# Optimization experiments

Hardware: AMD Instinct MI355X
Metric: run time of the kernel (lower is better)

## Reference

```python
import jax, jax.numpy as jnp
import numpy as np

B, S, H, NH, HD = 2, 2048, 2048, 16, 128
MASK_VALUE = -1e10


def setup_inputs() -> dict:
    key = jax.random.key(0)
    ks = jax.random.split(key, 5)
    scale = 1.0 / np.sqrt(H)
    x = jax.random.normal(ks[0], (B, S, H), dtype=jnp.float32)
    Wq = jax.random.normal(ks[1], (H, NH * HD), dtype=jnp.float32) * scale
    Wk = jax.random.normal(ks[2], (H, NH * HD), dtype=jnp.float32) * scale
    Wv = jax.random.normal(ks[3], (H, NH * HD), dtype=jnp.float32) * scale
    Wo = jax.random.normal(ks[4], (NH * HD, H), dtype=jnp.float32) * scale
    # causal boolean mask (B, S, S) as in decoder-style gemma usage
    mask = jnp.broadcast_to(jnp.tril(jnp.ones((S, S), dtype=bool)), (B, S, S))
    return {"x": x, "mask": mask, "Wq": Wq, "Wk": Wk, "Wv": Wv, "Wo": Wo}


def reference(x, mask, Wq, Wk, Wv, Wo):
    b, s, h = x.shape
    # bias-free QKV projections, split into heads -> (b, nh, s, hd)
    def split_heads(y):
        return y.reshape(b, s, NH, HD).transpose(0, 2, 1, 3)
    q = split_heads(x @ Wq)
    k = split_heads(x @ Wk)
    v = split_heads(x @ Wv)
    scores = jnp.einsum('bhtd,bhTd->bhtT', q, k) / jnp.sqrt(jnp.asarray(HD, x.dtype))
    scores = jnp.where(mask[:, None, :, :], scores, MASK_VALUE)
    weights = jax.nn.softmax(scores, axis=-1)
    out = jnp.einsum('bhtT,bhTd->bhtd', weights, v)
    out = out.transpose(0, 2, 1, 3).reshape(b, s, NH * HD)
    return out @ Wo
```

## Files before the change

kernel.cpp:

```cpp
#include <hip/hip_runtime.h>
#include <hip/hip_bf16.h>
#include <stdint.h>

#define DEVFN __device__ __forceinline__

typedef __attribute__((ext_vector_type(8))) short short8;
typedef __attribute__((ext_vector_type(4))) float f32x4;
typedef __attribute__((ext_vector_type(16))) float f32x16;

constexpr int S_LEN = 2048;
constexpr int HDIM  = 2048;
constexpr int NHEAD = 16;
constexpr int HD    = 128;

DEVFN unsigned short f2bf(float f){
  union { float f; unsigned u; } x; x.f = f;
  unsigned r = x.u + 0x7fffu + ((x.u >> 16) & 1u);
  return (unsigned short)(r >> 16);
}

typedef const __attribute__((address_space(1))) void* gas1_ptr;
typedef __attribute__((address_space(3))) void* las3_ptr;

DEVFN void gl_lds16(const void* g, void* l){
  __builtin_amdgcn_global_load_lds((gas1_ptr)g, (las3_ptr)l, 16, 0, 0);
}

DEVFN f32x4 mfma16(short8 a, short8 b, f32x4 c){
  return __builtin_amdgcn_mfma_f32_16x16x32_bf16(a, b, c, 0, 0, 0);
}

DEVFN f32x16 mfma32(short8 a, short8 b, f32x16 c){
  return __builtin_amdgcn_mfma_f32_32x32x16_bf16(a, b, c, 0, 0, 0);
}

DEVFN unsigned cvtpk_bf16(float lo, float hi){
  unsigned w;
  asm("v_cvt_pk_bf16_f32 %0, %1, %2" : "=v"(w) : "v"(lo), "v"(hi));
  return w;
}


__global__ void cast_x_kernel(const float* __restrict__ in, unsigned short* __restrict__ out){
  int i = (blockIdx.x * 256 + threadIdx.x) * 8;
  float4 a = *(const float4*)(in + i);
  float4 b = *(const float4*)(in + i + 4);
  union { unsigned short s[8]; short8 v; } o;
  o.s[0] = f2bf(a.x); o.s[1] = f2bf(a.y); o.s[2] = f2bf(a.z); o.s[3] = f2bf(a.w);
  o.s[4] = f2bf(b.x); o.s[5] = f2bf(b.y); o.s[6] = f2bf(b.z); o.s[7] = f2bf(b.w);
  *(short8*)(out + i) = o.v;
}

__global__ void transpose_cast_w4(const float* __restrict__ w0, const float* __restrict__ w1,
                                  const float* __restrict__ w2, const float* __restrict__ w3,
                                  unsigned short* __restrict__ out){
  __shared__ float tile[64][65];
  const int tid = threadIdx.x;
  const int kb = blockIdx.x * 64, nb = blockIdx.y * 64, z = blockIdx.z;
  const float* in = (z == 0) ? w0 : (z == 1) ? w1 : (z == 2) ? w2 : w3;
  unsigned short* op = out + (size_t)z * HDIM * HDIM;

  const int rr = tid >> 5;
  const int cc = (tid & 31) * 2;
  #pragma unroll
  for (int i = 0; i < 8; i++){
    int r = i*8 + rr;
    float2 v = *(const float2*)(in + (size_t)(kb + r) * HDIM + nb + cc);
    tile[r][cc]   = v.x;
    tile[r][cc+1] = v.y;
  }
  __syncthreads();
  #pragma unroll
  for (int p = 0; p < 2; p++){
    int task = p*256 + tid;
    int n_l = task >> 3;
    int k8  = (task & 7) * 8;
    union { unsigned short s[8]; short8 v; } o;
    #pragma unroll
    for (int j = 0; j < 8; j++)
      o.s[j] = f2bf(tile[k8 + j][n_l]);
    *(short8*)(op + (size_t)(nb + n_l) * HDIM + kb + k8) = o.v;
  }
}


DEVFN void gemm_core_bt(const unsigned short* __restrict__ A,
                        const unsigned short* __restrict__ Bt,
                        int K, int m0, int n0, char* ls, f32x4 (&acc)[4][4]){
  const int t = threadIdx.x;
  const int wid = t >> 6, lane = t & 63;
  const int wr = wid >> 1, wc = wid & 1;
  const int l15 = lane & 15, lg = lane >> 4;
  char* lsA = ls;
  char* lsB = ls + 16384;

  for (int k0 = 0; k0 < K; k0 += 64){
    __syncthreads();
    #pragma unroll
    for (int i = 0; i < 4; i++){
      int o = (t + i*256) * 16;
      int row = o >> 7;
      int col = (o & 127) ^ ((row & 7) << 4);
      gl_lds16((const char*)A + ((size_t)(m0 + row) * K + k0) * 2 + col, lsA + o);
    }
    #pragma unroll
    for (int i = 0; i < 4; i++){
      int o = (t + i*256) * 16;
      int row = o >> 7;
      int col = (o & 127) ^ ((row & 7) << 4);
      gl_lds16((const char*)Bt + ((size_t)(n0 + row) * K + k0) * 2 + col, lsB + o);
    }
    __syncthreads();
    #pragma unroll
    for (int kk = 0; kk < 2; kk++){
      short8 af[4], bfr[4];
      #pragma unroll
      for (int i = 0; i < 4; i++){
        int ra = wr*64 + i*16 + l15;
        af[i]  = *(const short8*)(lsA + ra*128 + ((kk*64 + lg*16) ^ ((ra & 7) << 4)));
        int rb = wc*64 + i*16 + l15;
        bfr[i] = *(const short8*)(lsB + rb*128 + ((kk*64 + lg*16) ^ ((rb & 7) << 4)));
      }
      #pragma unroll
      for (int i = 0; i < 4; i++)
        #pragma unroll
        for (int j = 0; j < 4; j++)
          acc[i][j] = mfma16(af[i], bfr[j], acc[i][j]);
    }
  }
}

__global__ __launch_bounds__(256, 4)
void gemm_qkv(const unsigned short* __restrict__ xb, const unsigned short* __restrict__ Wt,
              unsigned short* __restrict__ Qb, unsigned short* __restrict__ Kb,
              unsigned short* __restrict__ Vt){
  __shared__ __align__(16) char ls[32768];
  f32x4 acc[4][4];
  const f32x4 z4 = {0.f, 0.f, 0.f, 0.f};
  #pragma unroll
  for (int i = 0; i < 4; i++)
    #pragma unroll
    for (int j = 0; j < 4; j++) acc[i][j] = z4;

  const int m0 = blockIdx.x * 128;
  const int n0 = blockIdx.y * 128;
  gemm_core_bt(xb, Wt, HDIM, m0, n0, ls, acc);

  const float qscale = 0.08838834764831845f * 1.4426950408889634f;
  const int t = threadIdx.x, wid = t >> 6, lane = t & 63;
  const int wr = wid >> 1, wc = wid & 1, l15 = lane & 15, lg = lane >> 4;
  const int bb = m0 >> 11, ss0 = m0 & 2047;

  if (n0 < 4096){
    unsigned short* base = (n0 < 2048) ? Qb : Kb;
    const float sc = (n0 < 2048) ? qscale : 1.0f;
    #pragma unroll
    for (int j = 0; j < 4; j++){
      int n = n0 + wc*64 + j*16 + l15;
      int hh = (n >> 7) & 15, d = n & 127;
      #pragma unroll
      for (int i = 0; i < 4; i++){
        #pragma unroll
        for (int r = 0; r < 4; r++){
          int ss = ss0 + wr*64 + i*16 + lg*4 + r;
          base[(((size_t)bb * NHEAD + hh) * S_LEN + ss) * HD + d] = f2bf(acc[i][j][r] * sc);
        }
      }
    }
  } else {
    const int hh = (n0 - 4096) >> 7;
    __syncthreads();
    #pragma unroll
    for (int j = 0; j < 4; j++){
      int nn = wc*64 + j*16 + l15;
      #pragma unroll
      for (int i = 0; i < 4; i++){
        int mmb = (wr*64 + i*16 + lg*4) * 2;
        unsigned w0 = cvtpk_bf16(acc[i][j][0], acc[i][j][1]);
        unsigned w1 = cvtpk_bf16(acc[i][j][2], acc[i][j][3]);
        *(unsigned*)(ls + nn*256 + ((mmb    ) ^ ((nn & 7) << 4))) = w0;
        *(unsigned*)(ls + nn*256 + ((mmb + 4) ^ ((nn & 7) << 4))) = w1;
      }
    }
    __syncthreads();
    unsigned short* vout = Vt + (((size_t)bb * NHEAD + hh) * HD) * S_LEN;
    #pragma unroll
    for (int p = 0; p < 8; p++){
      int idx = p*256 + t;
      int d = idx >> 4;
      int m8 = (idx & 15) * 8;
      short8 v = *(const short8*)(ls + d*256 + ((m8*2) ^ ((d & 7) << 4)));
      *(short8*)(vout + (size_t)d * S_LEN + ss0 + m8) = v;
    }
  }
}

__global__ __launch_bounds__(256, 4)
void gemm_out(const unsigned short* __restrict__ Ob, const unsigned short* __restrict__ Wot,
              float* __restrict__ out){
  __shared__ __align__(16) char ls[32768];
  f32x4 acc[4][4];
  const f32x4 z4 = {0.f, 0.f, 0.f, 0.f};
  #pragma unroll
  for (int i = 0; i < 4; i++)
    #pragma unroll
    for (int j = 0; j < 4; j++) acc[i][j] = z4;

  const int m0 = blockIdx.x * 128;
  const int n0 = blockIdx.y * 128;
  gemm_core_bt(Ob, Wot, HDIM, m0, n0, ls, acc);

  const int t = threadIdx.x, wid = t >> 6, lane = t & 63;
  const int wr = wid >> 1, wc = wid & 1, l15 = lane & 15, lg = lane >> 4;
  #pragma unroll
  for (int i = 0; i < 4; i++){
    #pragma unroll
    for (int r = 0; r < 4; r++){
      int m = m0 + wr*64 + i*16 + lg*4 + r;
      #pragma unroll
      for (int j = 0; j < 4; j++){
        int n = n0 + wc*64 + j*16 + l15;
        out[(size_t)m * HDIM + n] = acc[i][j][r];
      }
    }
  }
}

__global__ __launch_bounds__(256, 2)
void attn_kernel(const unsigned short* __restrict__ Q,
                 const unsigned short* __restrict__ Kg,
                 const unsigned short* __restrict__ Vt,
                 unsigned short* __restrict__ Ob){
  __shared__ __align__(16) unsigned short Kl[2][64*128];
  __shared__ __align__(16) unsigned short Vl[3][128*64];

  const int t = threadIdx.x;
  const int wid = t >> 6, lane = t & 63;
  const int l31 = lane & 31, hi = lane >> 5;
  const int L = blockIdx.x;
  const int bh = L & 31;
  const int z = L >> 5;
  const int qt = (z < 8) ? z : 23 - z;
  const int b = bh >> 4, h = bh & 15;
  const unsigned short* Qp = Q  + (size_t)bh * S_LEN * HD;
  const unsigned short* Kp = Kg + (size_t)bh * S_LEN * HD;
  const unsigned short* Vp = Vt + (size_t)bh * S_LEN * HD;
  const int q0 = qt * 128;
  const int wrow0 = q0 + wid * 32;
  const int qrow = wrow0 + l31;
  const int nt = 2 * qt + 2;
  const int ntw = (wrow0 >> 6) + 1;

  auto stage = [&](int tdx){
    char* kb = (char*)&Kl[tdx & 1][0];
    char* vb = (char*)&Vl[tdx % 3][0];
    const int k0 = tdx * 64;
    #pragma unroll
    for (int i = 0; i < 4; i++){
      int o = (t + i*256) * 16;
      int row = o >> 8;
      int col = (o & 255) ^ ((row & 15) << 4);
      gl_lds16((const char*)(Kp + (size_t)(k0 + row) * HD) + col, kb + o);
    }
    #pragma unroll
    for (int i = 0; i < 4; i++){
      int o = (t + i*256) * 16;
      int row = o >> 7;
      int col = (o & 127) ^ ((row & 7) << 4);
      gl_lds16((const char*)(Vp + (size_t)row * S_LEN + k0) + col, vb + o);
    }
  };

  short8 qf[8];
  #pragma unroll
  for (int dk = 0; dk < 8; dk++)
    qf[dk] = *(const short8*)(Qp + (size_t)qrow * HD + dk*16 + hi*8);

  f32x16 oacc[4];
  #pragma unroll
  for (int db = 0; db < 4; db++)
    #pragma unroll
    for (int r = 0; r < 16; r++) oacc[db][r] = 0.f;
  float mrun = -1e30f, lsum = 0.f;
  short8 paA[4], paB[4];

  auto do_pv = [&](short8 (&pprev)[4], const char* vb){
    __builtin_amdgcn_s_setprio(1);
    #pragma unroll
    for (int ks = 0; ks < 4; ks++){
      #pragma unroll
      for (int db = 0; db < 4; db++){
        int vr = db*32 + l31;
        short8 vf = *(const short8*)(vb + vr*128 + ((ks*32 + hi*16) ^ ((vr & 7) << 4)));
        oacc[db] = mfma32(vf, pprev[ks], oacc[db]);
      }
    }
    __builtin_amdgcn_s_setprio(0);
  };

  auto body = [&](int tdx, short8 (&pcur)[4], short8 (&pprev)[4]){
    if (tdx + 1 < nt) stage(tdx + 1);
    const char* Kb_ = (const char*)&Kl[tdx & 1][0];
    const bool doQK = (tdx < ntw);
    const bool doPV = (tdx >= 1) && (tdx <= ntw);

    f32x16 sacc[2];
    if (doQK){
      #pragma unroll
      for (int cb = 0; cb < 2; cb++)
        #pragma unroll
        for (int r = 0; r < 16; r++) sacc[cb][r] = 0.f;
      __builtin_amdgcn_s_setprio(1);
      #pragma unroll
      for (int dk = 0; dk < 8; dk++){
        #pragma unroll
        for (int cb = 0; cb < 2; cb++){
          int kr = cb*32 + l31;
          short8 af = *(const short8*)(Kb_ + kr*256 + ((dk*32 + hi*16) ^ ((kr & 15) << 4)));
          sacc[cb] = mfma32(af, qf[dk], sacc[cb]);
        }
      }
      __builtin_amdgcn_s_setprio(0);
    }

    if (doPV) do_pv(pprev, (const char*)&Vl[(tdx - 1) % 3][0]);

    if (doQK){
      const int k0 = tdx * 64;
      if (tdx == ntw - 1){
        #pragma unroll
        for (int cb = 0; cb < 2; cb++)
          #pragma unroll
          for (int r = 0; r < 16; r++){
            int kcol = k0 + cb*32 + (r & 3) + 8*(r >> 2) + 4*hi;
            if (kcol > qrow) sacc[cb][r] = -1e30f;
          }
      }
      float mv[8];
      #pragma unroll
      for (int i = 0; i < 8; i++)
        mv[i] = fmaxf(fmaxf(sacc[0][i], sacc[0][i+8]), fmaxf(sacc[1][i], sacc[1][i+8]));
      #pragma unroll
      for (int s = 4; s > 0; s >>= 1)
        #pragma unroll
        for (int i = 0; i < 4; i++)
          if (i < s) mv[i] = fmaxf(mv[i], mv[i+s]);
      float mx = fmaxf(mv[0], __shfl_xor(mv[0], 32, 64));
      if (!__all(mx <= mrun + 8.f)){
        float mnew = fmaxf(mrun, mx);
        float alpha = exp2f(mrun - mnew);
        mrun = mnew;
        lsum *= alpha;
        #pragma unroll
        for (int db = 0; db < 4; db++)
          #pragma unroll
          for (int r = 0; r < 16; r++) oacc[db][r] *= alpha;
      }
      float ls = 0.f;
      #pragma unroll
      for (int cb = 0; cb < 2; cb++)
        #pragma unroll
        for (int r = 0; r < 16; r++){
          float p = exp2f(sacc[cb][r] - mrun);
          sacc[cb][r] = p;
          ls += p;
        }
      lsum += ls;
      #pragma unroll
      for (int ks = 0; ks < 4; ks++){
        int cb = ks >> 1, bs = (ks & 1) * 8;
        unsigned B1 = cvtpk_bf16(sacc[cb][bs+0], sacc[cb][bs+1]);
        unsigned B2 = cvtpk_bf16(sacc[cb][bs+2], sacc[cb][bs+3]);
        unsigned A1 = cvtpk_bf16(sacc[cb][bs+4], sacc[cb][bs+5]);
        unsigned A2 = cvtpk_bf16(sacc[cb][bs+6], sacc[cb][bs+7]);
        asm("v_permlane32_swap_b32 %0, %1" : "+v"(B1), "+v"(A1));
        asm("v_permlane32_swap_b32 %0, %1" : "+v"(B2), "+v"(A2));
        union { unsigned u[4]; short8 v; } pk;
        pk.u[0] = B1; pk.u[1] = B2; pk.u[2] = A1; pk.u[3] = A2;
        pcur[ks] = pk.v;
      }
    }

    asm volatile("s_waitcnt vmcnt(0)" ::: "memory");
    __builtin_amdgcn_s_barrier();
  };

  stage(0);
  asm volatile("s_waitcnt vmcnt(0)" ::: "memory");
  __builtin_amdgcn_s_barrier();

  #pragma unroll 1
  for (int tt = 0; tt < nt; tt += 2){
    body(tt,     paA, paB);
    body(tt + 1, paB, paA);
  }
  if (ntw == nt) do_pv(paB, (const char*)&Vl[(nt - 1) % 3][0]);

  float lt = lsum + __shfl_xor(lsum, 32, 64);
  float inv = 1.f / lt;
  #pragma unroll
  for (int db = 0; db < 4; db++)
    #pragma unroll
    for (int r = 0; r < 16; r++) oacc[db][r] *= inv;

  __builtin_amdgcn_s_barrier();
  char* reg_lds = (char*)&Kl[0][0] + wid * 8192;
  #pragma unroll
  for (int ms = 0; ms < 8; ms++){
    int db = ms >> 1, bs = (ms & 1) * 8;
    unsigned B1 = cvtpk_bf16(oacc[db][bs+0], oacc[db][bs+1]);
    unsigned B2 = cvtpk_bf16(oacc[db][bs+2], oacc[db][bs+3]);
    unsigned A1 = cvtpk_bf16(oacc[db][bs+4], oacc[db][bs+5]);
    unsigned A2 = cvtpk_bf16(oacc[db][bs+6], oacc[db][bs+7]);
    asm("v_permlane32_swap_b32 %0, %1" : "+v"(B1), "+v"(A1));
    asm("v_permlane32_swap_b32 %0, %1" : "+v"(B2), "+v"(A2));
    union { unsigned u[4]; short8 v; } pk;
    pk.u[0] = B1; pk.u[1] = B2; pk.u[2] = A1; pk.u[3] = A2;
    int byteo = l31*256 + ((ms*32 + hi*16) ^ ((l31 & 7) << 4));
    *(short8*)(reg_lds + byteo) = pk.v;
  }
  #pragma unroll
  for (int i = 0; i < 8; i++){
    int r = (lane >> 4) + i*4;
    int c = lane & 15;
    short8 v = *(const short8*)(reg_lds + r*256 + ((c*16) ^ ((r & 7) << 4)));
    *(short8*)(Ob + ((size_t)(b * S_LEN + wrow0 + r)) * 2048 + h*128 + c*8) = v;
  }
}

extern "C" void kernel_launch(void* const* d_in, const int* in_sizes, int n_in,
                              void* d_out, int out_size, void* d_ws, size_t ws_size,
                              hipStream_t stream){
  const float* x  = (const float*)d_in[0];
  const float* Wq = (const float*)d_in[2];
  const float* Wk = (const float*)d_in[3];
  const float* Wv = (const float*)d_in[4];
  const float* Wo = (const float*)d_in[5];

  char* ws = (char*)d_ws;
  unsigned short* xb  = (unsigned short*)(ws);
  unsigned short* Wt  = (unsigned short*)(ws + 16777216);
  unsigned short* Wot = (unsigned short*)(ws + 41943040);
  unsigned short* Qb  = (unsigned short*)(ws + 50331648);
  unsigned short* Kb  = (unsigned short*)(ws + 67108864);
  unsigned short* Vt  = (unsigned short*)(ws + 83886080);
  unsigned short* Ob  = xb;

  cast_x_kernel<<<4096, 256, 0, stream>>>(x, xb);
  transpose_cast_w4<<<dim3(32, 32, 4), 256, 0, stream>>>(Wq, Wk, Wv, Wo, Wt);

  gemm_qkv<<<dim3(32, 48), 256, 0, stream>>>(xb, Wt, Qb, Kb, Vt);

  attn_kernel<<<512, 256, 0, stream>>>(Qb, Kb, Vt, Ob);

  gemm_out<<<dim3(32, 16), 256, 0, stream>>>(Ob, Wot, (float*)d_out);
}
```

Baseline: 221.3 us.

## Pair causal q-tiles in one 512-thread block sharing K/V staging

Attention blocks now hold 8 waves: the first four handle q-tile p and the last four handle q-tile 15-p, with both groups sharing one staged K/V stream that runs the length of the longer tile. This halves the K/V global-to-LDS traffic per pair and balances causal work evenly across the 256 blocks. In exchange, occupancy drops to one block per CU with a larger LDS footprint, and the short-tile waves sit idle at barriers while the long tile finishes.

```diff
diff --git a/kernel.cpp b/kernel.cpp
--- a/kernel.cpp
+++ b/kernel.cpp
@@ -226,45 +226,46 @@
   }
 }
 
-__global__ __launch_bounds__(256, 2)
+__global__ __launch_bounds__(512, 1)
 void attn_kernel(const unsigned short* __restrict__ Q,
                  const unsigned short* __restrict__ Kg,
                  const unsigned short* __restrict__ Vt,
                  unsigned short* __restrict__ Ob){
-  __shared__ __align__(16) unsigned short Kl[2][64*128];
-  __shared__ __align__(16) unsigned short Vl[3][128*64];
+  __shared__ __align__(16) char LSD[81920];
+  char* const KlB = LSD;
+  char* const VlB = LSD + 32768;
 
   const int t = threadIdx.x;
   const int wid = t >> 6, lane = t & 63;
   const int l31 = lane & 31, hi = lane >> 5;
   const int L = blockIdx.x;
   const int bh = L & 31;
-  const int z = L >> 5;
-  const int qt = (z < 8) ? z : 23 - z;
+  const int p = L >> 5;
+  const int g = wid >> 2, wq = wid & 3;
+  const int qt = g ? (15 - p) : p;
   const int b = bh >> 4, h = bh & 15;
   const unsigned short* Qp = Q  + (size_t)bh * S_LEN * HD;
   const unsigned short* Kp = Kg + (size_t)bh * S_LEN * HD;
   const unsigned short* Vp = Vt + (size_t)bh * S_LEN * HD;
-  const int q0 = qt * 128;
-  const int wrow0 = q0 + wid * 32;
+  const int wrow0 = qt * 128 + wq * 32;
   const int qrow = wrow0 + l31;
-  const int nt = 2 * qt + 2;
+  const int nt = 2 * (15 - p) + 2;
   const int ntw = (wrow0 >> 6) + 1;
 
   auto stage = [&](int tdx){
-    char* kb = (char*)&Kl[tdx & 1][0];
-    char* vb = (char*)&Vl[tdx % 3][0];
+    char* kb = KlB + (tdx & 1) * 16384;
+    char* vb = VlB + (tdx % 3) * 16384;
     const int k0 = tdx * 64;
     #pragma unroll
-    for (int i = 0; i < 4; i++){
-      int o = (t + i*256) * 16;
+    for (int i = 0; i < 2; i++){
+      int o = (t + i*512) * 16;
       int row = o >> 8;
       int col = (o & 255) ^ ((row & 15) << 4);
       gl_lds16((const char*)(Kp + (size_t)(k0 + row) * HD) + col, kb + o);
     }
     #pragma unroll
-    for (int i = 0; i < 4; i++){
-      int o = (t + i*256) * 16;
+    for (int i = 0; i < 2; i++){
+      int o = (t + i*512) * 16;
       int row = o >> 7;
       int col = (o & 127) ^ ((row & 7) << 4);
       gl_lds16((const char*)(Vp + (size_t)row * S_LEN + k0) + col, vb + o);
@@ -300,7 +301,7 @@
 
   auto body = [&](int tdx, short8 (&pcur)[4], short8 (&pprev)[4]){
     if (tdx + 1 < nt) stage(tdx + 1);
-    const char* Kb_ = (const char*)&Kl[tdx & 1][0];
+    const char* Kb_ = KlB + (tdx & 1) * 16384;
     const bool doQK = (tdx < ntw);
     const bool doPV = (tdx >= 1) && (tdx <= ntw);
 
@@ -323,7 +324,7 @@
       __builtin_amdgcn_s_setprio(0);
     }
 
-    if (doPV) do_pv(pprev, (const char*)&Vl[(tdx - 1) % 3][0]);
+    if (doPV) do_pv(pprev, VlB + ((tdx - 1) % 3) * 16384);
 
     if (doQK){
       const int k0 = tdx * 64;
@@ -361,9 +362,9 @@
       for (int cb = 0; cb < 2; cb++)
         #pragma unroll
         for (int r = 0; r < 16; r++){
-          float p = exp2f(sacc[cb][r] - mrun);
-          sacc[cb][r] = p;
-          ls += p;
+          float pp = exp2f(sacc[cb][r] - mrun);
+          sacc[cb][r] = pp;
+          ls += pp;
         }
       lsum += ls;
       #pragma unroll
@@ -381,20 +382,18 @@
       }
     }
 
-    asm volatile("s_waitcnt vmcnt(0)" ::: "memory");
-    __builtin_amdgcn_s_barrier();
+    __syncthreads();
   };
 
   stage(0);
-  asm volatile("s_waitcnt vmcnt(0)" ::: "memory");
-  __builtin_amdgcn_s_barrier();
+  __syncthreads();
 
   #pragma unroll 1
   for (int tt = 0; tt < nt; tt += 2){
     body(tt,     paA, paB);
     body(tt + 1, paB, paA);
   }
-  if (ntw == nt) do_pv(paB, (const char*)&Vl[(nt - 1) % 3][0]);
+  if (ntw == nt) do_pv(paB, VlB + ((nt - 1) % 3) * 16384);
 
   float lt = lsum + __shfl_xor(lsum, 32, 64);
   float inv = 1.f / lt;
@@ -403,8 +402,8 @@
     #pragma unroll
     for (int r = 0; r < 16; r++) oacc[db][r] *= inv;
 
-  __builtin_amdgcn_s_barrier();
-  char* reg_lds = (char*)&Kl[0][0] + wid * 8192;
+  __syncthreads();
+  char* reg_lds = LSD + wid * 8192;
   #pragma unroll
   for (int ms = 0; ms < 8; ms++){
     int db = ms >> 1, bs = (ms & 1) * 8;
@@ -451,7 +450,7 @@
 
   gemm_qkv<<<dim3(32, 48), 256, 0, stream>>>(xb, Wt, Qb, Kb, Vt);
 
-  attn_kernel<<<512, 256, 0, stream>>>(Qb, Kb, Vt, Ob);
+  attn_kernel<<<256, 512, 0, stream>>>(Qb, Kb, Vt, Ob);
 
   gemm_out<<<dim3(32, 16), 256, 0, stream>>>(Ob, Wot, (float*)d_out);
 }
```

Measured after the change: 218.8 us (median of 4 runs). Within noise of the previous version (-1.1%).
